# Optimization experiments

Measured on AMD Instinct MI355X. Metric: run time of the kernel, lower is better.

## Reference

```python
import jax, jax.numpy as jnp
import numpy as np

NUM_SEQS = 128
TOTAL_TOKENS = 65536
HIDDEN = 768
FF = 3072
EPS = 1e-12  # torch F.normalize default eps


def _make_prompt_lens(rng: np.random.Generator) -> np.ndarray:
    # Ragged lengths in [64, 960], adjusted so they sum exactly to TOTAL_TOKENS.
    lens = rng.integers(64, 960, size=NUM_SEQS).astype(np.int64)
    lens = np.maximum(1, (lens * (TOTAL_TOKENS / lens.sum())).astype(np.int64))
    lens[-1] += TOTAL_TOKENS - lens.sum()
    assert lens.sum() == TOTAL_TOKENS and (lens > 0).all()
    return lens


def setup_inputs() -> dict:
    key = jax.random.key(0)
    k1, k2, k3 = jax.random.split(key, 3)
    hidden_states = jax.random.normal(k1, (TOTAL_TOKENS, HIDDEN), dtype=jnp.float32)
    prompt_lens = jnp.asarray(_make_prompt_lens(np.random.default_rng(0)))
    W1 = jax.random.normal(k2, (FF, HIDDEN), dtype=jnp.float32) * (HIDDEN ** -0.5)
    W2 = jax.random.normal(k3, (HIDDEN, FF), dtype=jnp.float32) * (FF ** -0.5)
    return {"hidden_states": hidden_states, "prompt_lens": prompt_lens, "W1": W1, "W2": W2}


def reference(hidden_states, prompt_lens, W1, W2):
    # hidden_states: [T, H]; prompt_lens: [S] summing to T.
    T = hidden_states.shape[0]
    S = prompt_lens.shape[0]
    # segment id of each token: index of first cumsum strictly greater than position
    seg_ids = jnp.searchsorted(jnp.cumsum(prompt_lens), jnp.arange(T), side="right")
    sums = jax.ops.segment_sum(hidden_states, seg_ids, num_segments=S)  # [S, H]
    pooled = sums / prompt_lens[:, None].astype(hidden_states.dtype)     # mean pool
    h = jnp.einsum("sh,fh->sf", pooled, W1)   # dense1: 768 -> 3072 (no bias)
    h = jnp.einsum("sf,hf->sh", h, W2)        # dense2: 3072 -> 768 (no bias)
    norm = jnp.linalg.norm(h, ord=2, axis=-1, keepdims=True)
    return h / jnp.maximum(norm, EPS)         # L2 normalize, [S, H]
```

## Files before the change

### kernel.cpp

```cpp
#include <hip/hip_runtime.h>

#define TOK   65536
#define HID   768
#define NSEQ  128
#define FFD   3072
#define CHUNK 64
#define NCHUNK (TOK / CHUNK)
#define KS1 5
#define KS2 20
#define KCH 160

__device__ __forceinline__ void add4(float4& a, const float4 b) {
  a.x += b.x; a.y += b.y; a.z += b.z; a.w += b.w;
}

__global__ __launch_bounds__(256) void prep_kernel(
    const int* __restrict__ lens, int* __restrict__ incl,
    int* __restrict__ start_seg) {
  __shared__ int sc[NSEQ];
  const int t = threadIdx.x;
  if (t < NSEQ) sc[t] = lens[t];
  __syncthreads();
  for (int off = 1; off < NSEQ; off <<= 1) {
    int v = 0;
    if (t < NSEQ && t >= off) v = sc[t - off];
    __syncthreads();
    if (t < NSEQ) sc[t] += v;
    __syncthreads();
  }
  if (t < NSEQ) incl[t] = sc[t];
  for (int c = t; c < NCHUNK; c += 256) {
    const int t0 = c * CHUNK;
    int lo = 0, hi = NSEQ - 1;
    while (lo < hi) { int mid = (lo + hi) >> 1; if (sc[mid] <= t0) lo = mid + 1; else hi = mid; }
    start_seg[c] = lo;
  }
}

__global__ __launch_bounds__(192) void pool_kernel(
    const float* __restrict__ x, const int* __restrict__ lens,
    const int* __restrict__ incl, const int* __restrict__ start_seg,
    float* __restrict__ pooled) {
  const int t0 = blockIdx.x * CHUNK;
  const int t1 = t0 + CHUNK;
  const int col = threadIdx.x;

  int seg = start_seg[blockIdx.x];
  int L = lens[seg];
  int cum = incl[seg] - L;

  const float4* xv = (const float4*)x + col;
  int t = t0;
  while (t < t1) {
    const int seg_end = cum + L;
    const int run_end = seg_end < t1 ? seg_end : t1;
    const int n = run_end - t;
    const float4* p = xv + (size_t)t * (HID / 4);
    float4 a0 = make_float4(0.f,0.f,0.f,0.f), a1 = a0, a2 = a0, a3 = a0;
    int i = 0;
    for (; i + 4 <= n; i += 4) {
      add4(a0, p[(size_t)(i+0) * (HID/4)]);
      add4(a1, p[(size_t)(i+1) * (HID/4)]);
      add4(a2, p[(size_t)(i+2) * (HID/4)]);
      add4(a3, p[(size_t)(i+3) * (HID/4)]);
    }
    for (; i < n; ++i) add4(a0, p[(size_t)i * (HID/4)]);
    add4(a0, a1); add4(a2, a3); add4(a0, a2);

    const float inv = 1.0f / (float)L;
    float* dst = pooled + (size_t)seg * HID + col * 4;
    atomicAdd(dst + 0, a0.x * inv);
    atomicAdd(dst + 1, a0.y * inv);
    atomicAdd(dst + 2, a0.z * inv);
    atomicAdd(dst + 3, a0.w * inv);

    t = run_end;
    if (run_end == seg_end) {
      cum = seg_end; ++seg;
      if (seg < NSEQ) L = lens[seg];
    }
  }
}

__global__ __launch_bounds__(256) void gemm_nt(
    const float* __restrict__ A, const float* __restrict__ B,
    float* __restrict__ Cp, int N, int Kt, int nsum, int pstride) {
  __shared__ float As[16][132];
  __shared__ float Bs[16][68];

  const int tid = threadIdx.x;
  const int f0 = blockIdx.x * 64;
  const int k0 = blockIdx.y * KCH;
  const int kend = (k0 + KCH) < Kt ? (k0 + KCH) : Kt;
  float* C = Cp + (size_t)blockIdx.y * NSEQ * N;
  const int fx = (tid & 15) * 4;
  const int sy = (tid >> 4) * 8;

  float acc[8][4];
  #pragma unroll
  for (int i = 0; i < 8; ++i)
    #pragma unroll
    for (int j = 0; j < 4; ++j) acc[i][j] = 0.f;

  for (int kc = k0; kc < kend; kc += 16) {
    #pragma unroll
    for (int r = 0; r < 2; ++r) {
      const int l = tid + 256 * r;
      const int s = l >> 2, k4 = (l & 3) * 4;
      const float* ap = A + (size_t)s * Kt + kc + k4;
      float4 v = *(const float4*)ap;
      for (int p = 1; p < nsum; ++p) {
        const float4 w = *(const float4*)(ap + (size_t)p * pstride);
        add4(v, w);
      }
      As[k4 + 0][s] = v.x; As[k4 + 1][s] = v.y;
      As[k4 + 2][s] = v.z; As[k4 + 3][s] = v.w;
    }
    {
      const int f = tid >> 2, k4 = (tid & 3) * 4;
      const float4 v = *(const float4*)(B + (size_t)(f0 + f) * Kt + kc + k4);
      Bs[k4 + 0][f] = v.x; Bs[k4 + 1][f] = v.y;
      Bs[k4 + 2][f] = v.z; Bs[k4 + 3][f] = v.w;
    }
    __syncthreads();
    #pragma unroll
    for (int kk = 0; kk < 16; ++kk) {
      const float4 aA = *(const float4*)&As[kk][sy];
      const float4 aB = *(const float4*)&As[kk][sy + 4];
      const float4 bb = *(const float4*)&Bs[kk][fx];
      acc[0][0] += aA.x*bb.x; acc[0][1] += aA.x*bb.y; acc[0][2] += aA.x*bb.z; acc[0][3] += aA.x*bb.w;
      acc[1][0] += aA.y*bb.x; acc[1][1] += aA.y*bb.y; acc[1][2] += aA.y*bb.z; acc[1][3] += aA.y*bb.w;
      acc[2][0] += aA.z*bb.x; acc[2][1] += aA.z*bb.y; acc[2][2] += aA.z*bb.z; acc[2][3] += aA.z*bb.w;
      acc[3][0] += aA.w*bb.x; acc[3][1] += aA.w*bb.y; acc[3][2] += aA.w*bb.z; acc[3][3] += aA.w*bb.w;
      acc[4][0] += aB.x*bb.x; acc[4][1] += aB.x*bb.y; acc[4][2] += aB.x*bb.z; acc[4][3] += aB.x*bb.w;
      acc[5][0] += aB.y*bb.x; acc[5][1] += aB.y*bb.y; acc[5][2] += aB.y*bb.z; acc[5][3] += aB.y*bb.w;
      acc[6][0] += aB.z*bb.x; acc[6][1] += aB.z*bb.y; acc[6][2] += aB.z*bb.z; acc[6][3] += aB.z*bb.w;
      acc[7][0] += aB.w*bb.x; acc[7][1] += aB.w*bb.y; acc[7][2] += aB.w*bb.z; acc[7][3] += aB.w*bb.w;
    }
    __syncthreads();
  }
  #pragma unroll
  for (int i = 0; i < 8; ++i) {
    float4 o = make_float4(acc[i][0], acc[i][1], acc[i][2], acc[i][3]);
    *(float4*)(C + (size_t)(sy + i) * N + f0 + fx) = o;
  }
}

__global__ __launch_bounds__(256) void norm_kernel(
    const float* __restrict__ outp, float* __restrict__ out) {
  const int s = blockIdx.x;
  const int tid = threadIdx.x;
  float v[3];
  #pragma unroll
  for (int j = 0; j < 3; ++j) {
    const int c = tid + 256 * j;
    float a = 0.f;
    for (int p = 0; p < KS2; ++p)
      a += outp[((size_t)p * NSEQ + s) * HID + c];
    v[j] = a;
  }
  float ss = v[0]*v[0] + v[1]*v[1] + v[2]*v[2];
  #pragma unroll
  for (int off = 32; off > 0; off >>= 1) ss += __shfl_down(ss, off, 64);
  __shared__ float wsum[4];
  if ((tid & 63) == 0) wsum[tid >> 6] = ss;
  __syncthreads();
  const float tot = wsum[0] + wsum[1] + wsum[2] + wsum[3];
  const float scale = 1.0f / fmaxf(sqrtf(tot), 1e-12f);
  #pragma unroll
  for (int j = 0; j < 3; ++j) out[(size_t)s * HID + tid + 256 * j] = v[j] * scale;
}

extern "C" void kernel_launch(void* const* d_in, const int* in_sizes, int n_in,
                              void* d_out, int out_size, void* d_ws, size_t ws_size,
                              hipStream_t stream) {
  const float* x    = (const float*)d_in[0];
  const int*   lens = (const int*)d_in[1];
  const float* W1   = (const float*)d_in[2];
  const float* W2   = (const float*)d_in[3];
  float* out = (float*)d_out;

  float* pooled = (float*)d_ws;
  float* h1p    = pooled + NSEQ * HID;
  float* outp   = h1p + (size_t)KS1 * NSEQ * FFD;
  int*   incl   = (int*)(outp + (size_t)KS2 * NSEQ * HID);
  int*   start_seg = incl + NSEQ;

  hipMemsetAsync(pooled, 0, (size_t)NSEQ * HID * sizeof(float), stream);

  prep_kernel<<<1, 256, 0, stream>>>(lens, incl, start_seg);
  pool_kernel<<<NCHUNK, 192, 0, stream>>>(x, lens, incl, start_seg, pooled);
  gemm_nt<<<dim3(FFD / 64, KS1), 256, 0, stream>>>(pooled, W1, h1p, FFD, HID, 1, 0);
  gemm_nt<<<dim3(HID / 64, KS2), 256, 0, stream>>>(h1p, W2, outp, HID, FFD, KS1, NSEQ * FFD);
  norm_kernel<<<NSEQ, 256, 0, stream>>>(outp, out);
}
```

Before: 355.1 us.

## Fuse pooling, both GEMMs and normalize into one cooperative kernel

Replaces the memset, prefix-scan, pooling, two split-K GEMM and normalize launches with a single cooperative kernel of 256 blocks that uses grid-wide syncs between stages. Every block recomputes the length prefix sum in shared memory, and the pooling stage now processes 4 chunks per block with 8 accumulators. The aim is to remove launch overhead and inter-kernel gaps. In exchange, pooling runs with only 256 blocks instead of 1024, so its memory parallelism may be lower, and the grid syncs add their own cost.

```diff
diff --git a/kernel.cpp b/kernel.cpp
--- a/kernel.cpp
+++ b/kernel.cpp
@@ -1,98 +1,30 @@
 #include <hip/hip_runtime.h>
+#include <hip/hip_cooperative_groups.h>
+namespace cg = cooperative_groups;
 
 #define TOK   65536
 #define HID   768
 #define NSEQ  128
 #define FFD   3072
 #define CHUNK 64
-#define NCHUNK (TOK / CHUNK)
-#define KS1 5
-#define KS2 20
-#define KCH 160
+#define CPB   4
+#define GRID  256
+#define KCH   160
+#define KS1   5
+#define KS2   20
 
 __device__ __forceinline__ void add4(float4& a, const float4 b) {
   a.x += b.x; a.y += b.y; a.z += b.z; a.w += b.w;
 }
 
-__global__ __launch_bounds__(256) void prep_kernel(
-    const int* __restrict__ lens, int* __restrict__ incl,
-    int* __restrict__ start_seg) {
-  __shared__ int sc[NSEQ];
-  const int t = threadIdx.x;
-  if (t < NSEQ) sc[t] = lens[t];
-  __syncthreads();
-  for (int off = 1; off < NSEQ; off <<= 1) {
-    int v = 0;
-    if (t < NSEQ && t >= off) v = sc[t - off];
-    __syncthreads();
-    if (t < NSEQ) sc[t] += v;
-    __syncthreads();
-  }
-  if (t < NSEQ) incl[t] = sc[t];
-  for (int c = t; c < NCHUNK; c += 256) {
-    const int t0 = c * CHUNK;
-    int lo = 0, hi = NSEQ - 1;
-    while (lo < hi) { int mid = (lo + hi) >> 1; if (sc[mid] <= t0) lo = mid + 1; else hi = mid; }
-    start_seg[c] = lo;
-  }
-}
-
-__global__ __launch_bounds__(192) void pool_kernel(
-    const float* __restrict__ x, const int* __restrict__ lens,
-    const int* __restrict__ incl, const int* __restrict__ start_seg,
-    float* __restrict__ pooled) {
-  const int t0 = blockIdx.x * CHUNK;
-  const int t1 = t0 + CHUNK;
-  const int col = threadIdx.x;
-
-  int seg = start_seg[blockIdx.x];
-  int L = lens[seg];
-  int cum = incl[seg] - L;
-
-  const float4* xv = (const float4*)x + col;
-  int t = t0;
-  while (t < t1) {
-    const int seg_end = cum + L;
-    const int run_end = seg_end < t1 ? seg_end : t1;
-    const int n = run_end - t;
-    const float4* p = xv + (size_t)t * (HID / 4);
-    float4 a0 = make_float4(0.f,0.f,0.f,0.f), a1 = a0, a2 = a0, a3 = a0;
-    int i = 0;
-    for (; i + 4 <= n; i += 4) {
-      add4(a0, p[(size_t)(i+0) * (HID/4)]);
-      add4(a1, p[(size_t)(i+1) * (HID/4)]);
-      add4(a2, p[(size_t)(i+2) * (HID/4)]);
-      add4(a3, p[(size_t)(i+3) * (HID/4)]);
-    }
-    for (; i < n; ++i) add4(a0, p[(size_t)i * (HID/4)]);
-    add4(a0, a1); add4(a2, a3); add4(a0, a2);
-
-    const float inv = 1.0f / (float)L;
-    float* dst = pooled + (size_t)seg * HID + col * 4;
-    atomicAdd(dst + 0, a0.x * inv);
-    atomicAdd(dst + 1, a0.y * inv);
-    atomicAdd(dst + 2, a0.z * inv);
-    atomicAdd(dst + 3, a0.w * inv);
-
-    t = run_end;
-    if (run_end == seg_end) {
-      cum = seg_end; ++seg;
-      if (seg < NSEQ) L = lens[seg];
-    }
-  }
-}
-
-__global__ __launch_bounds__(256) void gemm_nt(
-    const float* __restrict__ A, const float* __restrict__ B,
-    float* __restrict__ Cp, int N, int Kt, int nsum, int pstride) {
+template <int NSUM>
+__device__ void gemm_tile(const float* __restrict__ A, const float* __restrict__ B,
+                          float* __restrict__ C, int N, int Kt, int f0, int k0,
+                          int pstride, int tid) {
   __shared__ float As[16][132];
   __shared__ float Bs[16][68];
 
-  const int tid = threadIdx.x;
-  const int f0 = blockIdx.x * 64;
-  const int k0 = blockIdx.y * KCH;
   const int kend = (k0 + KCH) < Kt ? (k0 + KCH) : Kt;
-  float* C = Cp + (size_t)blockIdx.y * NSEQ * N;
   const int fx = (tid & 15) * 4;
   const int sy = (tid >> 4) * 8;
 
@@ -109,10 +41,8 @@
       const int s = l >> 2, k4 = (l & 3) * 4;
       const float* ap = A + (size_t)s * Kt + kc + k4;
       float4 v = *(const float4*)ap;
-      for (int p = 1; p < nsum; ++p) {
-        const float4 w = *(const float4*)(ap + (size_t)p * pstride);
-        add4(v, w);
-      }
+      #pragma unroll
+      for (int p = 1; p < NSUM; ++p) add4(v, *(const float4*)(ap + (size_t)p * pstride));
       As[k4 + 0][s] = v.x; As[k4 + 1][s] = v.y;
       As[k4 + 2][s] = v.z; As[k4 + 3][s] = v.w;
     }
@@ -140,35 +70,110 @@
     __syncthreads();
   }
   #pragma unroll
-  for (int i = 0; i < 8; ++i) {
-    float4 o = make_float4(acc[i][0], acc[i][1], acc[i][2], acc[i][3]);
-    *(float4*)(C + (size_t)(sy + i) * N + f0 + fx) = o;
-  }
+  for (int i = 0; i < 8; ++i)
+    *(float4*)(C + (size_t)(sy + i) * N + f0 + fx) =
+        make_float4(acc[i][0], acc[i][1], acc[i][2], acc[i][3]);
 }
 
-__global__ __launch_bounds__(256) void norm_kernel(
-    const float* __restrict__ outp, float* __restrict__ out) {
-  const int s = blockIdx.x;
+__global__ __launch_bounds__(256) void fused_kernel(
+    const float* __restrict__ x, const int* __restrict__ lens,
+    const float* __restrict__ W1, const float* __restrict__ W2,
+    float* __restrict__ out, float* __restrict__ pooled,
+    float* __restrict__ h1p, float* __restrict__ outp) {
+  cg::grid_group grid = cg::this_grid();
   const int tid = threadIdx.x;
-  float v[3];
-  #pragma unroll
-  for (int j = 0; j < 3; ++j) {
-    const int c = tid + 256 * j;
-    float a = 0.f;
-    for (int p = 0; p < KS2; ++p)
-      a += outp[((size_t)p * NSEQ + s) * HID + c];
-    v[j] = a;
+  const int b = blockIdx.x;
+  __shared__ int sc[NSEQ];
+  __shared__ float wsum[4];
+
+  if (b < 96) ((float4*)pooled)[b * 256 + tid] = make_float4(0.f, 0.f, 0.f, 0.f);
+  if (tid < NSEQ) sc[tid] = lens[tid];
+  __syncthreads();
+  for (int off = 1; off < NSEQ; off <<= 1) {
+    int v = 0;
+    if (tid < NSEQ && tid >= off) v = sc[tid - off];
+    __syncthreads();
+    if (tid < NSEQ) sc[tid] += v;
+    __syncthreads();
   }
-  float ss = v[0]*v[0] + v[1]*v[1] + v[2]*v[2];
-  #pragma unroll
-  for (int off = 32; off > 0; off >>= 1) ss += __shfl_down(ss, off, 64);
-  __shared__ float wsum[4];
-  if ((tid & 63) == 0) wsum[tid >> 6] = ss;
-  __syncthreads();
-  const float tot = wsum[0] + wsum[1] + wsum[2] + wsum[3];
-  const float scale = 1.0f / fmaxf(sqrtf(tot), 1e-12f);
-  #pragma unroll
-  for (int j = 0; j < 3; ++j) out[(size_t)s * HID + tid + 256 * j] = v[j] * scale;
+  grid.sync();
+
+  if (tid < 192) {
+    const int col = tid;
+    const float4* xv = (const float4*)x + col;
+    for (int c = 0; c < CPB; ++c) {
+      const int t0 = (b * CPB + c) * CHUNK;
+      const int t1 = t0 + CHUNK;
+      int lo = 0, hi = NSEQ - 1;
+      while (lo < hi) { int mid = (lo + hi) >> 1; if (sc[mid] <= t0) lo = mid + 1; else hi = mid; }
+      int seg = lo;
+      int segend = sc[seg];
+      int L = seg ? segend - sc[seg - 1] : segend;
+      int t = t0;
+      while (t < t1) {
+        const int run_end = segend < t1 ? segend : t1;
+        const int n = run_end - t;
+        const float4* p = xv + (size_t)t * (HID / 4);
+        float4 a0 = make_float4(0.f,0.f,0.f,0.f), a1 = a0, a2 = a0, a3 = a0,
+               a4 = a0, a5 = a0, a6 = a0, a7 = a0;
+        int i = 0;
+        for (; i + 8 <= n; i += 8) {
+          add4(a0, p[(size_t)(i+0) * 192]); add4(a1, p[(size_t)(i+1) * 192]);
+          add4(a2, p[(size_t)(i+2) * 192]); add4(a3, p[(size_t)(i+3) * 192]);
+          add4(a4, p[(size_t)(i+4) * 192]); add4(a5, p[(size_t)(i+5) * 192]);
+          add4(a6, p[(size_t)(i+6) * 192]); add4(a7, p[(size_t)(i+7) * 192]);
+        }
+        for (; i < n; ++i) add4(a0, p[(size_t)i * 192]);
+        add4(a0, a1); add4(a2, a3); add4(a4, a5); add4(a6, a7);
+        add4(a0, a2); add4(a4, a6); add4(a0, a4);
+
+        const float inv = 1.0f / (float)L;
+        float* dst = pooled + (size_t)seg * HID + col * 4;
+        atomicAdd(dst + 0, a0.x * inv);
+        atomicAdd(dst + 1, a0.y * inv);
+        atomicAdd(dst + 2, a0.z * inv);
+        atomicAdd(dst + 3, a0.w * inv);
+
+        t = run_end;
+        if (run_end == segend) {
+          ++seg;
+          if (seg < NSEQ) { const int pe = segend; segend = sc[seg]; L = segend - pe; }
+        }
+      }
+    }
+  }
+  grid.sync();
+
+  if (b < 48 * KS1)
+    gemm_tile<1>(pooled, W1, h1p + (size_t)(b / 48) * NSEQ * FFD,
+                 FFD, HID, (b % 48) * 64, (b / 48) * KCH, 0, tid);
+  grid.sync();
+
+  if (b < 12 * KS2)
+    gemm_tile<KS1>(h1p, W2, outp + (size_t)(b / 12) * NSEQ * HID,
+                   HID, FFD, (b % 12) * 64, (b / 12) * KCH, NSEQ * FFD, tid);
+  grid.sync();
+
+  if (b < NSEQ) {
+    const int s = b;
+    float v[3];
+    #pragma unroll
+    for (int j = 0; j < 3; ++j) {
+      const int cidx = tid + 256 * j;
+      float a = 0.f;
+      for (int p = 0; p < KS2; ++p) a += outp[((size_t)p * NSEQ + s) * HID + cidx];
+      v[j] = a;
+    }
+    float ss = v[0]*v[0] + v[1]*v[1] + v[2]*v[2];
+    #pragma unroll
+    for (int off = 32; off > 0; off >>= 1) ss += __shfl_down(ss, off, 64);
+    if ((tid & 63) == 0) wsum[tid >> 6] = ss;
+    __syncthreads();
+    const float tot = wsum[0] + wsum[1] + wsum[2] + wsum[3];
+    const float scale = 1.0f / fmaxf(sqrtf(tot), 1e-12f);
+    #pragma unroll
+    for (int j = 0; j < 3; ++j) out[(size_t)s * HID + tid + 256 * j] = v[j] * scale;
+  }
 }
 
 extern "C" void kernel_launch(void* const* d_in, const int* in_sizes, int n_in,
@@ -183,14 +188,9 @@
   float* pooled = (float*)d_ws;
   float* h1p    = pooled + NSEQ * HID;
   float* outp   = h1p + (size_t)KS1 * NSEQ * FFD;
-  int*   incl   = (int*)(outp + (size_t)KS2 * NSEQ * HID);
-  int*   start_seg = incl + NSEQ;
 
-  hipMemsetAsync(pooled, 0, (size_t)NSEQ * HID * sizeof(float), stream);
-
-  prep_kernel<<<1, 256, 0, stream>>>(lens, incl, start_seg);
-  pool_kernel<<<NCHUNK, 192, 0, stream>>>(x, lens, incl, start_seg, pooled);
-  gemm_nt<<<dim3(FFD / 64, KS1), 256, 0, stream>>>(pooled, W1, h1p, FFD, HID, 1, 0);
-  gemm_nt<<<dim3(HID / 64, KS2), 256, 0, stream>>>(h1p, W2, outp, HID, FFD, KS1, NSEQ * FFD);
-  norm_kernel<<<NSEQ, 256, 0, stream>>>(outp, out);
+  void* args[] = {(void*)&x, (void*)&lens, (void*)&W1, (void*)&W2,
+                  (void*)&out, (void*)&pooled, (void*)&h1p, (void*)&outp};
+  hipLaunchCooperativeKernel((void*)fused_kernel, dim3(GRID), dim3(256),
+                             args, 0, stream);
 }
```

Result: slower. 456.0 us (+28.4%).
